# Optimization experiments

Measured on AMD Instinct MI355X. Metric: run time of the kernel, lower is better.

Reference implementation:

```python
import jax, jax.numpy as jnp
import numpy as np

TOP_K = 2  # num_experts_per_tok


def setup_inputs() -> dict:
    key = jax.random.key(0)
    ks = jax.random.split(key, 5)
    B, T, D, E, F = 2, 2048, 1024, 8, 2048
    scale_d = 1.0 / np.sqrt(D)
    scale_f = 1.0 / np.sqrt(F)
    return {
        "x": jax.random.normal(ks[0], (B, T, D), jnp.float32),
        "kernel_router_DE": jax.random.normal(ks[1], (D, E), jnp.float32) * scale_d,
        "kernel_gating_EDF": jax.random.normal(ks[2], (E, D, F), jnp.float32) * scale_d,
        "kernel_up_EDF": jax.random.normal(ks[3], (E, D, F), jnp.float32) * scale_d,
        "kernel_down_EFD": jax.random.normal(ks[4], (E, F, D), jnp.float32) * scale_f,
    }


def reference(x, kernel_router_DE, kernel_gating_EDF, kernel_up_EDF, kernel_down_EFD):
    E = kernel_router_DE.shape[-1]
    x = x.astype(jnp.float32)

    # --- Router: logits -> softmax -> top_k -> renormalize with softmax ---
    router_logits_BTE = jnp.einsum('BTD,DE->BTE', x, kernel_router_DE)
    probs_BTE = jax.nn.softmax(router_logits_BTE.astype(jnp.float32), axis=-1)
    weights_BTX, indices_BTX = jax.lax.top_k(probs_BTE, TOP_K)
    norm_weights_BTX = jax.nn.softmax(weights_BTX, axis=-1)

    # --- Scatter top-k weights back to dense per-expert weights ---
    one_hot_BTXE = jax.nn.one_hot(indices_BTX, num_classes=E, dtype=jnp.float32)
    full_weights_BTE = jnp.sum(one_hot_BTXE * norm_weights_BTX[..., None], axis=2)

    # --- Dense all-expert MLP (gating * up -> down), weighted combine ---
    gating_BTEF = jnp.einsum('BTD,EDF->BTEF', x, kernel_gating_EDF)
    fuse_BTEF = jax.nn.silu(gating_BTEF) * jnp.einsum('BTD,EDF->BTEF', x, kernel_up_EDF)
    down_BTED = jnp.einsum('BTEF,EFD->BTED', fuse_BTEF, kernel_down_EFD)
    out_BTD = jnp.einsum('BTED,BTE->BTD', down_BTED, full_weights_BTE)
    return out_BTD.astype(jnp.float32)
```

## Files before the change

kernel.cpp:

```cpp
#include <hip/hip_runtime.h>
#include <cstdint>

#define N_TOK 4096
#define DIM   1024
#define NEXP  8
#define FDIM  2048

typedef _Float16 f16_t;
typedef _Float16 f16x8 __attribute__((ext_vector_type(8)));
typedef float    f32x4 __attribute__((ext_vector_type(4)));

__device__ inline unsigned packh(float a, float b) {
    union { f16_t h[2]; unsigned u; } p;
    p.h[0] = (f16_t)a; p.h[1] = (f16_t)b;
    return p.u;
}

__device__ inline void gl2lds16(const void* g, void* l) {
    __builtin_amdgcn_global_load_lds(
        (const __attribute__((address_space(1))) unsigned*)g,
        (__attribute__((address_space(3))) unsigned*)l, 16, 0, 0);
}

__global__ __launch_bounds__(256) void router_kernel(
    const float* __restrict__ x, const float* __restrict__ wr,
    float* __restrict__ topw, int* __restrict__ counts, int* __restrict__ bucket)
{
    __shared__ float r[NEXP][DIM];
    __shared__ int sIdx[32];
    int tid = threadIdx.x;
    for (int i = tid; i < DIM * NEXP / 4; i += 256) {
        float4 v = ((const float4*)wr)[i];
        int base = i * 4;
        r[(base + 0) & 7][(base + 0) >> 3] = v.x;
        r[(base + 1) & 7][(base + 1) >> 3] = v.y;
        r[(base + 2) & 7][(base + 2) >> 3] = v.z;
        r[(base + 3) & 7][(base + 3) >> 3] = v.w;
    }
    __syncthreads();
    int wave = tid >> 6, lane = tid & 63;
    int t0 = blockIdx.x * 16 + wave * 4;
    for (int tt = 0; tt < 4; ++tt) {
        int t = t0 + tt;
        float acc[NEXP];
#pragma unroll
        for (int e = 0; e < NEXP; e++) acc[e] = 0.f;
        const float* xr = x + (size_t)t * DIM;
#pragma unroll
        for (int k = 0; k < DIM / 64; k++) {
            int d = lane + k * 64;
            float xv = xr[d];
#pragma unroll
            for (int e = 0; e < NEXP; e++) acc[e] += xv * r[e][d];
        }
#pragma unroll
        for (int e = 0; e < NEXP; e++) {
#pragma unroll
            for (int off = 32; off > 0; off >>= 1)
                acc[e] += __shfl_xor(acc[e], off, 64);
        }
        if (lane == 0) {
            float mx = acc[0];
#pragma unroll
            for (int e = 1; e < NEXP; e++) mx = fmaxf(mx, acc[e]);
            float p[NEXP]; float s = 0.f;
#pragma unroll
            for (int e = 0; e < NEXP; e++) { p[e] = expf(acc[e] - mx); s += p[e]; }
            float inv = 1.f / s;
#pragma unroll
            for (int e = 0; e < NEXP; e++) p[e] *= inv;
            int i1 = 0; float p1 = p[0];
#pragma unroll
            for (int e = 1; e < NEXP; e++) if (p[e] > p1) { p1 = p[e]; i1 = e; }
            int i2 = -1; float p2 = -1.f;
#pragma unroll
            for (int e = 0; e < NEXP; e++) if (e != i1 && p[e] > p2) { p2 = p[e]; i2 = e; }
            float e2 = expf(p2 - p1);
            float w1 = 1.f / (1.f + e2);
            topw[t * 2 + 0] = w1;
            topw[t * 2 + 1] = e2 * w1;
            int j = (wave * 4 + tt) * 2;
            sIdx[j + 0] = i1;
            sIdx[j + 1] = i2;
        }
    }
    __syncthreads();
    if (tid < NEXP) {
        int cnt = 0;
#pragma unroll
        for (int j = 0; j < 32; j++) cnt += (sIdx[j] == tid) ? 1 : 0;
        if (cnt > 0) {
            int pos = atomicAdd(&counts[tid * 32], cnt);
#pragma unroll
            for (int j = 0; j < 32; j++)
                if (sIdx[j] == tid)
                    bucket[tid * N_TOK + pos++] = (blockIdx.x * 16 + (j >> 1)) * 2 + (j & 1);
        }
    }
}

__global__ __launch_bounds__(256) void xcast_kernel(const float* __restrict__ x, f16_t* __restrict__ xf)
{
    int i = blockIdx.x * 256 + threadIdx.x;
    float4 a = ((const float4*)x)[2 * i];
    float4 b = ((const float4*)x)[2 * i + 1];
    union { f16_t h[8]; uint4 u; } p;
    p.h[0] = (f16_t)a.x; p.h[1] = (f16_t)a.y; p.h[2] = (f16_t)a.z; p.h[3] = (f16_t)a.w;
    p.h[4] = (f16_t)b.x; p.h[5] = (f16_t)b.y; p.h[6] = (f16_t)b.z; p.h[7] = (f16_t)b.w;
    ((uint4*)xf)[i] = p.u;
}

__global__ __launch_bounds__(256) void transpose_cvt(
    const float* __restrict__ inA, const float* __restrict__ inB,
    f16_t* __restrict__ outA, f16_t* __restrict__ outB,
    int R, int C, int tiles_r, int nA)
{
    __shared__ unsigned sP[64][68];
    int m = blockIdx.y;
    const float* in; f16_t* out;
    if (m < nA) { in = inA + (size_t)m * DIM * FDIM; out = outA + (size_t)m * DIM * FDIM; }
    else        { in = inB + (size_t)(m - nA) * DIM * FDIM; out = outB + (size_t)(m - nA) * DIM * FDIM; }
    int tix = blockIdx.x;
    int rb = (tix % tiles_r) * 128;
    int cb = (tix / tiles_r) * 64;
    int t = threadIdx.x;
    int dp = t >> 2;
    int fc = (t & 3) * 16;
    const float* r0 = in + (size_t)(rb + 2 * dp) * C + cb + fc;
    const float* r1 = r0 + C;
#pragma unroll
    for (int j = 0; j < 16; j += 4) {
        float4 a = *(const float4*)(r0 + j);
        float4 b = *(const float4*)(r1 + j);
        sP[fc + j + 0][dp] = packh(a.x, b.x);
        sP[fc + j + 1][dp] = packh(a.y, b.y);
        sP[fc + j + 2][dp] = packh(a.z, b.z);
        sP[fc + j + 3][dp] = packh(a.w, b.w);
    }
    __syncthreads();
    int c = t >> 2;
    int rc = t & 3;
    uint4* dst = (uint4*)(out + (size_t)(cb + c) * R + rb + rc * 32);
    const unsigned* src = &sP[c][rc * 16];
#pragma unroll
    for (int j = 0; j < 4; j++)
        dst[j] = *(const uint4*)(src + j * 4);
}

__global__ __launch_bounds__(256) void gateup_kernel(
    const f16_t* __restrict__ xf,
    const f16_t* __restrict__ wgT, const f16_t* __restrict__ wuT,
    const int* __restrict__ counts, const int* __restrict__ bucket,
    f16_t* __restrict__ H)
{
    int e = blockIdx.z;
    int cnt = counts[e * 32];
    int m0 = blockIdx.y * 128;
    if (m0 >= cnt) return;
    int n0 = blockIdx.x * 64;

    __shared__ f16_t sA[128 * 32];
    __shared__ f16_t sBg[64 * 32];
    __shared__ f16_t sBu[64 * 32];
    __shared__ int sEnt[128];

    int tid = threadIdx.x;
    if (tid < 128) {
        int i = m0 + tid;
        sEnt[tid] = bucket[e * N_TOK + (i < cnt ? i : m0)];
    }
    __syncthreads();

    int wave = tid >> 6, lane = tid & 63;
    int q = ((lane & 3) - (lane >> 3)) & 3;
    int rA0 = wave * 32 + (lane >> 2);
    int rA1 = rA0 + 16;
    int rB  = wave * 16 + (lane >> 2);
    const f16_t* gA0 = xf + (size_t)(sEnt[rA0] >> 1) * DIM + q * 8;
    const f16_t* gA1 = xf + (size_t)(sEnt[rA1] >> 1) * DIM + q * 8;
    const f16_t* gBg = wgT + ((size_t)e * FDIM + n0 + rB) * DIM + q * 8;
    const f16_t* gBu = wuT + ((size_t)e * FDIM + n0 + rB) * DIM + q * 8;
    f16_t* lA0 = &sA[wave * 1024 + lane * 8];
    f16_t* lA1 = lA0 + 512;
    f16_t* lBg = &sBg[wave * 512 + lane * 8];
    f16_t* lBu = &sBu[wave * 512 + lane * 8];

    f32x4 accG[4][2], accU[4][2];
    f32x4 zero = {0.f, 0.f, 0.f, 0.f};
#pragma unroll
    for (int i = 0; i < 4; i++)
#pragma unroll
        for (int j = 0; j < 2; j++) { accG[i][j] = zero; accU[i][j] = zero; }

    int wm = (wave & 1) * 64, wn = (wave >> 1) * 32;
    int fm = lane & 15, quad = lane >> 4;
    int p8 = ((quad + (fm >> 1)) & 3) * 8;

    for (int k0 = 0; k0 < DIM; k0 += 32) {
        gl2lds16(gA0 + k0, lA0);
        gl2lds16(gA1 + k0, lA1);
        gl2lds16(gBg + k0, lBg);
        gl2lds16(gBu + k0, lBu);
        __syncthreads();
        f16x8 af[4], bg[2], bu[2];
#pragma unroll
        for (int mi = 0; mi < 4; mi++)
            af[mi] = *(const f16x8*)&sA[(wm + mi * 16 + fm) * 32 + p8];
#pragma unroll
        for (int ni = 0; ni < 2; ni++) {
            bg[ni] = *(const f16x8*)&sBg[(wn + ni * 16 + fm) * 32 + p8];
            bu[ni] = *(const f16x8*)&sBu[(wn + ni * 16 + fm) * 32 + p8];
        }
#pragma unroll
        for (int mi = 0; mi < 4; mi++)
#pragma unroll
            for (int ni = 0; ni < 2; ni++) {
                accG[mi][ni] = __builtin_amdgcn_mfma_f32_16x16x32_f16(af[mi], bg[ni], accG[mi][ni], 0, 0, 0);
                accU[mi][ni] = __builtin_amdgcn_mfma_f32_16x16x32_f16(af[mi], bu[ni], accU[mi][ni], 0, 0, 0);
            }
        __syncthreads();
    }
    int crow = quad * 4, ccol = fm;
#pragma unroll
    for (int mi = 0; mi < 4; mi++) {
#pragma unroll
        for (int i = 0; i < 4; i++) {
            int m = wm + mi * 16 + crow + i;
            if (m0 + m < cnt) {
                int ent = sEnt[m];
                f16_t* hr = H + (size_t)ent * FDIM + n0 + wn;
#pragma unroll
                for (int ni = 0; ni < 2; ni++) {
                    float g = accG[mi][ni][i], u = accU[mi][ni][i];
                    float h = (g / (1.f + __expf(-g))) * u;
                    hr[ni * 16 + ccol] = (f16_t)h;
                }
            }
        }
    }
}

__global__ __launch_bounds__(256) void down_kernel(
    const f16_t* __restrict__ H, const f16_t* __restrict__ wdT,
    const int* __restrict__ counts, const int* __restrict__ bucket,
    const float* __restrict__ topw, float* __restrict__ Y)
{
    int e = blockIdx.z;
    int cnt = counts[e * 32];
    int m0 = blockIdx.y * 128;
    if (m0 >= cnt) return;
    int n0 = blockIdx.x * 128;

    __shared__ f16_t sA[128 * 32];
    __shared__ f16_t sB[128 * 32];
    __shared__ int sEnt[128];

    int tid = threadIdx.x;
    if (tid < 128) {
        int i = m0 + tid;
        sEnt[tid] = bucket[e * N_TOK + (i < cnt ? i : m0)];
    }
    __syncthreads();

    int wave = tid >> 6, lane = tid & 63;
    int q = ((lane & 3) - (lane >> 3)) & 3;
    int r0 = wave * 32 + (lane >> 2);
    int r1 = r0 + 16;
    const f16_t* gA0 = H + (size_t)sEnt[r0] * FDIM + q * 8;
    const f16_t* gA1 = H + (size_t)sEnt[r1] * FDIM + q * 8;
    const f16_t* gB0 = wdT + ((size_t)e * DIM + n0 + r0) * FDIM + q * 8;
    const f16_t* gB1 = wdT + ((size_t)e * DIM + n0 + r1) * FDIM + q * 8;
    f16_t* lA0 = &sA[wave * 1024 + lane * 8];
    f16_t* lA1 = lA0 + 512;
    f16_t* lB0 = &sB[wave * 1024 + lane * 8];
    f16_t* lB1 = lB0 + 512;

    f32x4 acc[4][4];
    f32x4 zero = {0.f, 0.f, 0.f, 0.f};
#pragma unroll
    for (int i = 0; i < 4; i++)
#pragma unroll
        for (int j = 0; j < 4; j++) acc[i][j] = zero;

    int wm = (wave & 1) * 64, wn = (wave >> 1) * 64;
    int fm = lane & 15, quad = lane >> 4;
    int p8 = ((quad + (fm >> 1)) & 3) * 8;

    for (int k0 = 0; k0 < FDIM; k0 += 32) {
        gl2lds16(gA0 + k0, lA0);
        gl2lds16(gA1 + k0, lA1);
        gl2lds16(gB0 + k0, lB0);
        gl2lds16(gB1 + k0, lB1);
        __syncthreads();
        f16x8 af[4], bf[4];
#pragma unroll
        for (int mi = 0; mi < 4; mi++)
            af[mi] = *(const f16x8*)&sA[(wm + mi * 16 + fm) * 32 + p8];
#pragma unroll
        for (int ni = 0; ni < 4; ni++)
            bf[ni] = *(const f16x8*)&sB[(wn + ni * 16 + fm) * 32 + p8];
#pragma unroll
        for (int mi = 0; mi < 4; mi++)
#pragma unroll
            for (int ni = 0; ni < 4; ni++)
                acc[mi][ni] = __builtin_amdgcn_mfma_f32_16x16x32_f16(af[mi], bf[ni], acc[mi][ni], 0, 0, 0);
        __syncthreads();
    }
    int crow = quad * 4, ccol = fm;
#pragma unroll
    for (int mi = 0; mi < 4; mi++) {
#pragma unroll
        for (int i = 0; i < 4; i++) {
            int m = wm + mi * 16 + crow + i;
            if (m0 + m < cnt) {
                int ent = sEnt[m];
                float w = topw[ent];
                float* yr = Y + (size_t)ent * DIM + n0 + wn;
#pragma unroll
                for (int ni = 0; ni < 4; ni++)
                    yr[ni * 16 + ccol] = w * acc[mi][ni][i];
            }
        }
    }
}

__global__ __launch_bounds__(256) void combine_kernel(
    const float* __restrict__ Y, float* __restrict__ out)
{
    int i = blockIdx.x * 256 + threadIdx.x;
    int t = i >> 8;
    int c = i & 255;
    float4 a = ((const float4*)Y)[(size_t)(2 * t) * 256 + c];
    float4 b = ((const float4*)Y)[(size_t)(2 * t + 1) * 256 + c];
    float4 o;
    o.x = a.x + b.x; o.y = a.y + b.y; o.z = a.z + b.z; o.w = a.w + b.w;
    ((float4*)out)[i] = o;
}

extern "C" void kernel_launch(void* const* d_in, const int* in_sizes, int n_in,
                              void* d_out, int out_size, void* d_ws, size_t ws_size,
                              hipStream_t stream) {
    const float* x  = (const float*)d_in[0];
    const float* wr = (const float*)d_in[1];
    const float* wg = (const float*)d_in[2];
    const float* wu = (const float*)d_in[3];
    const float* wd = (const float*)d_in[4];
    float* out = (float*)d_out;
    char* ws = (char*)d_ws;
    const size_t MB = 1ull << 20;

    int*   counts = (int*)ws;
    int*   bucket = (int*)(ws + 1024);
    float* topw   = (float*)(ws + 160 * 1024);
    f16_t* xf     = (f16_t*)(ws + 1 * MB);
    f16_t* wgT    = (f16_t*)(ws + 9 * MB);
    f16_t* wuT    = (f16_t*)(ws + 41 * MB);
    f16_t* H      = (f16_t*)(ws + 73 * MB);
    f16_t* wdT    = (f16_t*)(ws + 1 * MB);
    float* Y      = (float*)(ws + 33 * MB);

    hipMemsetAsync(counts, 0, 1024, stream);
    router_kernel<<<256, 256, 0, stream>>>(x, wr, topw, counts, bucket);
    xcast_kernel<<<2048, 256, 0, stream>>>(x, xf);
    transpose_cvt<<<dim3(256, 16), 256, 0, stream>>>(wg, wu, wgT, wuT, DIM, FDIM, DIM / 128, NEXP);
    gateup_kernel<<<dim3(FDIM / 64, 32, NEXP), 256, 0, stream>>>(xf, wgT, wuT, counts, bucket, H);
    transpose_cvt<<<dim3(256, 8), 256, 0, stream>>>(wd, wd, wdT, wdT, FDIM, DIM, FDIM / 128, NEXP);
    down_kernel<<<dim3(DIM / 128, 32, NEXP), 256, 0, stream>>>(H, wdT, counts, bucket, topw, Y);
    combine_kernel<<<4096, 256, 0, stream>>>(Y, out);
}
```

Measured before the change: 416.1 us.

## Fuse router, x cast and weight transposes into one prep kernel

Merges the router, the fp16 cast of x and the gate/up (and, when workspace allows, down) weight transpose-converts into a single prep kernel that dispatches on block index. This removes several kernel launches and lets the router and transposes overlap. The routing weight is moved from the down epilogue into the gate/up epilogue, so it is applied to H before the fp16 store, which slightly changes rounding. The workspace layout is chosen by size so that wdT does not alias xf.

```diff
diff --git a/kernel.cpp b/kernel.cpp
--- a/kernel.cpp
+++ b/kernel.cpp
@@ -22,36 +22,89 @@
         (__attribute__((address_space(3))) unsigned*)l, 16, 0, 0);
 }
 
-__global__ __launch_bounds__(256) void router_kernel(
+__device__ void transpose_tile(const float* __restrict__ in, f16_t* __restrict__ out,
+                               int R, int C, int tiles_r, int tix, unsigned (*sP)[68])
+{
+    int rb = (tix % tiles_r) * 128;
+    int cb = (tix / tiles_r) * 64;
+    int t = threadIdx.x;
+    int dp = t >> 2;
+    int fc = (t & 3) * 16;
+    const float* r0 = in + (size_t)(rb + 2 * dp) * C + cb + fc;
+    const float* r1 = r0 + C;
+#pragma unroll
+    for (int j = 0; j < 16; j += 4) {
+        float4 a = *(const float4*)(r0 + j);
+        float4 b = *(const float4*)(r1 + j);
+        sP[fc + j + 0][dp] = packh(a.x, b.x);
+        sP[fc + j + 1][dp] = packh(a.y, b.y);
+        sP[fc + j + 2][dp] = packh(a.z, b.z);
+        sP[fc + j + 3][dp] = packh(a.w, b.w);
+    }
+    __syncthreads();
+    int c = t >> 2;
+    int rc = t & 3;
+    uint4* dst = (uint4*)(out + (size_t)(cb + c) * R + rb + rc * 32);
+    const unsigned* src = &sP[c][rc * 16];
+#pragma unroll
+    for (int j = 0; j < 4; j++)
+        dst[j] = *(const uint4*)(src + j * 4);
+}
+
+__global__ __launch_bounds__(256) void prep_kernel(
     const float* __restrict__ x, const float* __restrict__ wr,
+    const float* __restrict__ wg, const float* __restrict__ wu, const float* __restrict__ wd,
+    f16_t* __restrict__ xf, f16_t* __restrict__ wgT, f16_t* __restrict__ wuT, f16_t* __restrict__ wdT,
     float* __restrict__ topw, int* __restrict__ counts, int* __restrict__ bucket)
 {
-    __shared__ float r[NEXP][DIM];
+    __shared__ union { float r[NEXP][DIM]; unsigned sP[64][68]; } sh;
     __shared__ int sIdx[32];
+    int bx = blockIdx.x;
     int tid = threadIdx.x;
+
+    if (bx >= 256) {
+        if (bx < 256 + 4096) {
+            int tix = bx - 256;
+            int m = tix >> 8;
+            int tt = tix & 255;
+            const float* in = (m < 8) ? wg + (size_t)m * DIM * FDIM : wu + (size_t)(m - 8) * DIM * FDIM;
+            f16_t* out      = (m < 8) ? wgT + (size_t)m * DIM * FDIM : wuT + (size_t)(m - 8) * DIM * FDIM;
+            transpose_tile(in, out, DIM, FDIM, DIM / 128, tt, sh.sP);
+        } else {
+            int tix = bx - (256 + 4096);
+            int m = tix >> 8;
+            int tt = tix & 255;
+            transpose_tile(wd + (size_t)m * FDIM * DIM, wdT + (size_t)m * FDIM * DIM,
+                           FDIM, DIM, FDIM / 128, tt, sh.sP);
+        }
+        return;
+    }
+
     for (int i = tid; i < DIM * NEXP / 4; i += 256) {
         float4 v = ((const float4*)wr)[i];
         int base = i * 4;
-        r[(base + 0) & 7][(base + 0) >> 3] = v.x;
-        r[(base + 1) & 7][(base + 1) >> 3] = v.y;
-        r[(base + 2) & 7][(base + 2) >> 3] = v.z;
-        r[(base + 3) & 7][(base + 3) >> 3] = v.w;
+        sh.r[(base + 0) & 7][(base + 0) >> 3] = v.x;
+        sh.r[(base + 1) & 7][(base + 1) >> 3] = v.y;
+        sh.r[(base + 2) & 7][(base + 2) >> 3] = v.z;
+        sh.r[(base + 3) & 7][(base + 3) >> 3] = v.w;
     }
     __syncthreads();
     int wave = tid >> 6, lane = tid & 63;
-    int t0 = blockIdx.x * 16 + wave * 4;
+    int t0 = bx * 16 + wave * 4;
     for (int tt = 0; tt < 4; ++tt) {
         int t = t0 + tt;
         float acc[NEXP];
 #pragma unroll
         for (int e = 0; e < NEXP; e++) acc[e] = 0.f;
         const float* xr = x + (size_t)t * DIM;
+        f16_t* xo = xf + (size_t)t * DIM;
 #pragma unroll
         for (int k = 0; k < DIM / 64; k++) {
             int d = lane + k * 64;
             float xv = xr[d];
-#pragma unroll
-            for (int e = 0; e < NEXP; e++) acc[e] += xv * r[e][d];
+            xo[d] = (f16_t)xv;
+#pragma unroll
+            for (int e = 0; e < NEXP; e++) acc[e] += xv * sh.r[e][d];
         }
 #pragma unroll
         for (int e = 0; e < NEXP; e++) {
@@ -94,64 +147,26 @@
 #pragma unroll
             for (int j = 0; j < 32; j++)
                 if (sIdx[j] == tid)
-                    bucket[tid * N_TOK + pos++] = (blockIdx.x * 16 + (j >> 1)) * 2 + (j & 1);
-        }
-    }
-}
-
-__global__ __launch_bounds__(256) void xcast_kernel(const float* __restrict__ x, f16_t* __restrict__ xf)
-{
-    int i = blockIdx.x * 256 + threadIdx.x;
-    float4 a = ((const float4*)x)[2 * i];
-    float4 b = ((const float4*)x)[2 * i + 1];
-    union { f16_t h[8]; uint4 u; } p;
-    p.h[0] = (f16_t)a.x; p.h[1] = (f16_t)a.y; p.h[2] = (f16_t)a.z; p.h[3] = (f16_t)a.w;
-    p.h[4] = (f16_t)b.x; p.h[5] = (f16_t)b.y; p.h[6] = (f16_t)b.z; p.h[7] = (f16_t)b.w;
-    ((uint4*)xf)[i] = p.u;
-}
-
-__global__ __launch_bounds__(256) void transpose_cvt(
-    const float* __restrict__ inA, const float* __restrict__ inB,
-    f16_t* __restrict__ outA, f16_t* __restrict__ outB,
-    int R, int C, int tiles_r, int nA)
+                    bucket[tid * N_TOK + pos++] = (bx * 16 + (j >> 1)) * 2 + (j & 1);
+        }
+    }
+}
+
+__global__ __launch_bounds__(256) void transpose_d_kernel(
+    const float* __restrict__ wd, f16_t* __restrict__ wdT)
 {
     __shared__ unsigned sP[64][68];
-    int m = blockIdx.y;
-    const float* in; f16_t* out;
-    if (m < nA) { in = inA + (size_t)m * DIM * FDIM; out = outA + (size_t)m * DIM * FDIM; }
-    else        { in = inB + (size_t)(m - nA) * DIM * FDIM; out = outB + (size_t)(m - nA) * DIM * FDIM; }
-    int tix = blockIdx.x;
-    int rb = (tix % tiles_r) * 128;
-    int cb = (tix / tiles_r) * 64;
-    int t = threadIdx.x;
-    int dp = t >> 2;
-    int fc = (t & 3) * 16;
-    const float* r0 = in + (size_t)(rb + 2 * dp) * C + cb + fc;
-    const float* r1 = r0 + C;
-#pragma unroll
-    for (int j = 0; j < 16; j += 4) {
-        float4 a = *(const float4*)(r0 + j);
-        float4 b = *(const float4*)(r1 + j);
-        sP[fc + j + 0][dp] = packh(a.x, b.x);
-        sP[fc + j + 1][dp] = packh(a.y, b.y);
-        sP[fc + j + 2][dp] = packh(a.z, b.z);
-        sP[fc + j + 3][dp] = packh(a.w, b.w);
-    }
-    __syncthreads();
-    int c = t >> 2;
-    int rc = t & 3;
-    uint4* dst = (uint4*)(out + (size_t)(cb + c) * R + rb + rc * 32);
-    const unsigned* src = &sP[c][rc * 16];
-#pragma unroll
-    for (int j = 0; j < 4; j++)
-        dst[j] = *(const uint4*)(src + j * 4);
+    int m = blockIdx.x >> 8;
+    int tt = blockIdx.x & 255;
+    transpose_tile(wd + (size_t)m * FDIM * DIM, wdT + (size_t)m * FDIM * DIM,
+                   FDIM, DIM, FDIM / 128, tt, sP);
 }
 
 __global__ __launch_bounds__(256) void gateup_kernel(
     const f16_t* __restrict__ xf,
     const f16_t* __restrict__ wgT, const f16_t* __restrict__ wuT,
     const int* __restrict__ counts, const int* __restrict__ bucket,
-    f16_t* __restrict__ H)
+    const float* __restrict__ topw, f16_t* __restrict__ H)
 {
     int e = blockIdx.z;
     int cnt = counts[e * 32];
@@ -228,11 +243,12 @@
             int m = wm + mi * 16 + crow + i;
             if (m0 + m < cnt) {
                 int ent = sEnt[m];
+                float w = topw[ent];
                 f16_t* hr = H + (size_t)ent * FDIM + n0 + wn;
 #pragma unroll
                 for (int ni = 0; ni < 2; ni++) {
                     float g = accG[mi][ni][i], u = accU[mi][ni][i];
-                    float h = (g / (1.f + __expf(-g))) * u;
+                    float h = (g / (1.f + __expf(-g))) * u * w;
                     hr[ni * 16 + ccol] = (f16_t)h;
                 }
             }
@@ -243,7 +259,7 @@
 __global__ __launch_bounds__(256) void down_kernel(
     const f16_t* __restrict__ H, const f16_t* __restrict__ wdT,
     const int* __restrict__ counts, const int* __restrict__ bucket,
-    const float* __restrict__ topw, float* __restrict__ Y)
+    float* __restrict__ Y)
 {
     int e = blockIdx.z;
     int cnt = counts[e * 32];
@@ -314,11 +330,10 @@
             int m = wm + mi * 16 + crow + i;
             if (m0 + m < cnt) {
                 int ent = sEnt[m];
-                float w = topw[ent];
                 float* yr = Y + (size_t)ent * DIM + n0 + wn;
 #pragma unroll
                 for (int ni = 0; ni < 4; ni++)
-                    yr[ni * 16 + ccol] = w * acc[mi][ni][i];
+                    yr[ni * 16 + ccol] = acc[mi][ni][i];
             }
         }
     }
@@ -356,15 +371,25 @@
     f16_t* wgT    = (f16_t*)(ws + 9 * MB);
     f16_t* wuT    = (f16_t*)(ws + 41 * MB);
     f16_t* H      = (f16_t*)(ws + 73 * MB);
-    f16_t* wdT    = (f16_t*)(ws + 1 * MB);
-    float* Y      = (float*)(ws + 33 * MB);
+
+    bool big_ws = (ws_size >= 138 * MB);
+    f16_t* wdT;
+    float* Y;
+    if (big_ws) {
+        wdT = (f16_t*)(ws + 105 * MB);
+        Y   = (float*)(ws + 1 * MB);
+    } else {
+        wdT = (f16_t*)(ws + 1 * MB);
+        Y   = (float*)(ws + 33 * MB);
+    }
 
     hipMemsetAsync(counts, 0, 1024, stream);
-    router_kernel<<<256, 256, 0, stream>>>(x, wr, topw, counts, bucket);
-    xcast_kernel<<<2048, 256, 0, stream>>>(x, xf);
-    transpose_cvt<<<dim3(256, 16), 256, 0, stream>>>(wg, wu, wgT, wuT, DIM, FDIM, DIM / 128, NEXP);
-    gateup_kernel<<<dim3(FDIM / 64, 32, NEXP), 256, 0, stream>>>(xf, wgT, wuT, counts, bucket, H);
-    transpose_cvt<<<dim3(256, 8), 256, 0, stream>>>(wd, wd, wdT, wdT, FDIM, DIM, FDIM / 128, NEXP);
-    down_kernel<<<dim3(DIM / 128, 32, NEXP), 256, 0, stream>>>(H, wdT, counts, bucket, topw, Y);
+    int prep_blocks = 256 + 4096 + (big_ws ? 2048 : 0);
+    prep_kernel<<<prep_blocks, 256, 0, stream>>>(x, wr, wg, wu, wd,
+                                                 xf, wgT, wuT, wdT, topw, counts, bucket);
+    gateup_kernel<<<dim3(FDIM / 64, 32, NEXP), 256, 0, stream>>>(xf, wgT, wuT, counts, bucket, topw, H);
+    if (!big_ws)
+        transpose_d_kernel<<<2048, 256, 0, stream>>>(wd, wdT);
+    down_kernel<<<dim3(DIM / 128, 32, NEXP), 256, 0, stream>>>(H, wdT, counts, bucket, Y);
     combine_kernel<<<4096, 256, 0, stream>>>(Y, out);
 }
```

Result: slower. 447.9 us (+7.6%).
